# Kernel optimization log

Measured on AMD Instinct MI355X. Metric: run time of the kernel, lower is better.

The kernel has to match this reference:

```python
import jax, jax.numpy as jnp
import numpy as np

NUM_SLOTS = 64
MEMORY_DIM = 512
EMBED_DIM = 1024
SCALE = MEMORY_DIM ** (-0.5)


def setup_inputs() -> dict:
    key = jax.random.key(0)
    ks = jax.random.split(key, 7)
    B, S, E, Dm = 8, 4096, EMBED_DIM, MEMORY_DIM
    s = 0.02
    return {
        "embeddings": jax.random.normal(ks[0], (B, S, E), dtype=jnp.float32),
        "W_write": jax.random.normal(ks[1], (E, Dm), dtype=jnp.float32) * s,
        "b_write": jnp.zeros((Dm,), dtype=jnp.float32),
        "W_query": jax.random.normal(ks[2], (E, Dm), dtype=jnp.float32) * s,
        "b_query": jnp.zeros((Dm,), dtype=jnp.float32),
        "W_out": jax.random.normal(ks[3], (Dm, E), dtype=jnp.float32) * s,
        "b_out": jnp.zeros((E,), dtype=jnp.float32),
    }


def reference(embeddings, W_write, b_write, W_query, b_query, W_out, b_out):
    B, S, E = embeddings.shape
    M, Dm = NUM_SLOTS, MEMORY_DIM
    # Precompute per-token projections (linear, so identical to per-step).
    write_vals = jnp.einsum('bse,ed->bsd', embeddings, W_write) + b_write  # [B,S,Dm]
    queries = jnp.einsum('bse,ed->bsd', embeddings, W_query) + b_query      # [B,S,Dm]
    addrs = jnp.arange(S) % M  # hash(position) = position % M

    def step(carry, xs):
        memory, written = carry            # [B,M,Dm], [B,M] bool
        q, wv, addr = xs                   # [B,Dm], [B,Dm], scalar int
        # read BEFORE write (current token not yet in memory)
        sim = jnp.einsum('bd,bmd->bm', q, memory) * SCALE
        sim = jnp.where(written, sim, -jnp.inf)
        attn = jax.nn.softmax(sim, axis=-1)
        attn = jnp.nan_to_num(attn)        # all-unwritten -> zeros
        retrieved = jnp.einsum('bm,bmd->bd', attn, memory)
        memory = memory.at[:, addr, :].set(wv)
        written = written.at[:, addr].set(True)
        return (memory, written), retrieved

    mem0 = jnp.zeros((B, M, Dm), dtype=embeddings.dtype)
    wr0 = jnp.zeros((B, M), dtype=bool)
    xs = (queries.transpose(1, 0, 2), write_vals.transpose(1, 0, 2), addrs)
    _, retrieved = jax.lax.scan(step, (mem0, wr0), xs)  # [S,B,Dm]
    retrieved = retrieved.transpose(1, 0, 2)            # [B,S,Dm]
    # read_out is linear per-step -> apply once over the whole sequence
    return jnp.einsum('bsd,de->bse', retrieved, W_out) + b_out
```

## Files before the change

kernel.cpp:

```cpp
#include <hip/hip_runtime.h>
#include <hip/hip_bf16.h>
#include <math.h>


#define BATCH   8
#define S_LEN   4096
#define EMB     1024
#define DM      512
#define MROWS   (BATCH * S_LEN)
#define SCALE_F 0.04419417382415922f

typedef __attribute__((ext_vector_type(4))) float f32x4;
typedef __attribute__((ext_vector_type(8))) short short8;

__device__ __forceinline__ unsigned short f2bf(float f) {
    __hip_bfloat16 h = __float2bfloat16(f);
    return *reinterpret_cast<unsigned short*>(&h);
}

__global__ __launch_bounds__(256) void prep(
    const float4* __restrict__ emb4, ushort4* __restrict__ embb4,
    const float* __restrict__ W_wr, const float* __restrict__ W_qr,
    const float* __restrict__ W_out,
    const float* __restrict__ b_wr, const float* __restrict__ b_qr,
    __hip_bfloat16* __restrict__ wcat, __hip_bfloat16* __restrict__ wout,
    float* __restrict__ bcat)
{
    const int bx = blockIdx.x;
    if (bx < 32768) {
        int id = bx * 256 + threadIdx.x;
        float4 v = emb4[id];
        ushort4 o;
        o.x = f2bf(v.x); o.y = f2bf(v.y); o.z = f2bf(v.z); o.w = f2bf(v.w);
        embb4[id] = o;
    } else if (bx < 32768 + 2048) {
        int id = (bx - 32768) * 256 + threadIdx.x;
        int n = id >> 10, k = id & 1023;
        wcat[id] = __float2bfloat16(W_wr[k * 512 + n]);
    } else if (bx < 32768 + 4096) {
        int id = (bx - 32768 - 2048) * 256 + threadIdx.x;
        int n = id >> 10, k = id & 1023;
        wcat[(size_t)DM * EMB + id] = __float2bfloat16(W_qr[k * 512 + n]);
    } else if (bx < 32768 + 6144) {
        int id = (bx - 32768 - 4096) * 256 + threadIdx.x;
        int n = id >> 9, k = id & 511;
        wout[id] = __float2bfloat16(W_out[k * 1024 + n]);
    } else {
        int i = threadIdx.x;
#pragma unroll
        for (int r = 0; r < 4; ++r, i += 256)
            bcat[i] = (i < 512) ? b_wr[i] : b_qr[i - 512];
    }
}

template<bool BF16OUT>
__global__ __launch_bounds__(512, 2) void gemm256(
    const __hip_bfloat16* __restrict__ A, int lda,
    const __hip_bfloat16* __restrict__ Bt, int ldb,
    const float* __restrict__ bias,
    void* __restrict__ Cv, int ldc,
    int K, int nbx)
{
    __shared__ __align__(16) char smem[131072];

    const int nwg = gridDim.x;
    const int bid = blockIdx.x;
    const int cpx = nwg >> 3;
    const int swz = (bid & 7) * cpx + (bid >> 3);
    const int bm0 = (swz / nbx) << 8;
    const int bn0 = (swz % nbx) << 8;

    const int tid  = threadIdx.x;
    const int lane = tid & 63;
    const int w    = tid >> 6;
    const int wm   = w >> 2, wn = w & 3;
    const int l15  = lane & 15, lhi = lane >> 4;
    const int nt   = K >> 6;

    const int r64 = tid >> 3;
    const int cg8 = ((tid & 7) ^ (r64 & 7)) << 3;

    auto stage_tile = [&](int buf, int kt) {
#pragma unroll
        for (int h = 0; h < 4; ++h) {
            const int isB = h >> 1, hh = h & 1;
            const __hip_bfloat16* G = isB ? Bt : A;
            const int ldg = isB ? ldb : lda;
            const int rb  = (isB ? bn0 : bm0) + hh * 128;
#pragma unroll
            for (int i = 0; i < 2; ++i) {
                const __hip_bfloat16* g =
                    G + (size_t)(rb + i * 64 + r64) * ldg + kt + cg8;
                char* l = smem + buf * 65536 + isB * 32768 + hh * 16384
                          + i * 8192 + w * 1024;
                __builtin_amdgcn_global_load_lds(
                    (const __attribute__((address_space(1))) unsigned int*)g,
                    (__attribute__((address_space(3))) unsigned int*)l, 16, 0, 0);
            }
        }
    };

    f32x4 acc[8][4] = {};

    stage_tile(0, 0);
    __syncthreads();

    for (int t = 0; t < nt; ++t) {
        const int cur = t & 1;
        const bool pf = (t + 1 < nt);
        if (pf) stage_tile(cur ^ 1, (t + 1) << 6);

        const char* sA = smem + cur * 65536;
        const char* sB = sA + 32768;

        short8 bfv[2][2][2];
#pragma unroll
        for (int nh = 0; nh < 2; ++nh)
#pragma unroll
            for (int ni = 0; ni < 2; ++ni) {
                const int r = wn * 64 + nh * 32 + ni * 16 + l15;
#pragma unroll
                for (int kk = 0; kk < 2; ++kk) {
                    const int pc = (kk * 4 + lhi) ^ (r & 7);
                    bfv[nh][ni][kk] = *(const short8*)(sB + r * 128 + (pc << 4));
                }
            }

#pragma unroll
        for (int mh = 0; mh < 2; ++mh) {
            short8 af[4][2];
#pragma unroll
            for (int mi = 0; mi < 4; ++mi) {
                const int r = wm * 128 + mh * 64 + mi * 16 + l15;
#pragma unroll
                for (int kk = 0; kk < 2; ++kk) {
                    const int pc = (kk * 4 + lhi) ^ (r & 7);
                    af[mi][kk] = *(const short8*)(sA + r * 128 + (pc << 4));
                }
            }
#pragma unroll
            for (int nh = 0; nh < 2; ++nh)
#pragma unroll
                for (int mi = 0; mi < 4; ++mi)
#pragma unroll
                    for (int ni = 0; ni < 2; ++ni)
#pragma unroll
                        for (int kk = 0; kk < 2; ++kk)
                            acc[mh * 4 + mi][nh * 2 + ni] =
                                __builtin_amdgcn_mfma_f32_16x16x32_bf16(
                                    af[mi][kk], bfv[nh][ni][kk],
                                    acc[mh * 4 + mi][nh * 2 + ni], 0, 0, 0);
        }

        if (pf) __syncthreads();
    }

    float bv[4];
#pragma unroll
    for (int N = 0; N < 4; ++N)
        bv[N] = bias[bn0 + wn * 64 + (N >> 1) * 32 + (N & 1) * 16 + l15];

#pragma unroll
    for (int M = 0; M < 8; ++M)
#pragma unroll
        for (int N = 0; N < 4; ++N)
#pragma unroll
            for (int reg = 0; reg < 4; ++reg) {
                int row = bm0 + wm * 128 + (M >> 2) * 64 + (M & 3) * 16
                          + lhi * 4 + reg;
                int col = bn0 + wn * 64 + (N >> 1) * 32 + (N & 1) * 16 + l15;
                float v = acc[M][N][reg] + bv[N];
                if (BF16OUT)
                    ((__hip_bfloat16*)Cv)[(size_t)row * ldc + col] = __float2bfloat16(v);
                else
                    ((float*)Cv)[(size_t)row * ldc + col] = v;
            }
}

__global__ __launch_bounds__(256) void transpose_wv(
    const unsigned short* __restrict__ wvq,
    unsigned short* __restrict__ wvt)
{
    __shared__ unsigned short tl[64][66];
    const int tx  = blockIdx.x;
    const int dx  = blockIdx.y;
    const int b   = blockIdx.z;
    const int tid = threadIdx.x;
    const int r   = tid >> 3;
    const int c8  = (tid & 7) * 8;
    const size_t bbase = (size_t)b << 12;

#pragma unroll
    for (int it = 0; it < 2; ++it) {
        int row = r + it * 32;
        uint4 v = *(const uint4*)(wvq + ((bbase + tx * 64 + row) << 10) + dx * 64 + c8);
        *(unsigned*)&tl[row][c8 + 0] = v.x;
        *(unsigned*)&tl[row][c8 + 2] = v.y;
        *(unsigned*)&tl[row][c8 + 4] = v.z;
        *(unsigned*)&tl[row][c8 + 6] = v.w;
    }
    __syncthreads();
#pragma unroll
    for (int it = 0; it < 2; ++it) {
        int drow = r + it * 32;
        union { unsigned short s[8]; uint4 v; } o;
#pragma unroll
        for (int k = 0; k < 8; ++k) o.s[k] = tl[c8 + k][drow];
        *(uint4*)(wvt + (((size_t)b * 512 + dx * 64 + drow) << 12) + tx * 64 + c8) = o.v;
    }
}

__global__ __launch_bounds__(256) void attn_mfma(
    const __hip_bfloat16* __restrict__ WVQ,
    const __hip_bfloat16* __restrict__ WVT,
    __hip_bfloat16* __restrict__ R)
{
    __shared__ __align__(16) unsigned short p_lds[64][136];

    const int blk = blockIdx.x;
    const int b   = blk >> 6;
    const int t0  = (blk & 63) << 6;
    const int jmin = (t0 == 0) ? 64 : 0;
    const size_t bbase = (size_t)b << 12;
    const int tid  = threadIdx.x;
    const int lane = tid & 63;
    const int w    = tid >> 6;
    const int l15  = lane & 15;
    const int lhi  = lane >> 4;

    f32x4 acc[8] = {};
    const __hip_bfloat16* q0 =
        WVQ + ((bbase + t0 + w * 16 + l15) << 10) + 512 + lhi * 8;

    const __hip_bfloat16* brow[8];
#pragma unroll
    for (int nt = 0; nt < 8; ++nt) {
        int aj = t0 - 64 + nt * 16 + l15;
        if (aj < 0) aj = 0;
        brow[nt] = WVQ + ((bbase + aj) << 10) + lhi * 8;
    }

#pragma unroll 2
    for (int kt = 0; kt < 16; ++kt) {
        short8 qa = *(const short8*)(q0 + kt * 32);
#pragma unroll
        for (int nt = 0; nt < 8; ++nt) {
            short8 bv = *(const short8*)(brow[nt] + kt * 32);
            acc[nt] = __builtin_amdgcn_mfma_f32_16x16x32_bf16(qa, bv, acc[nt], 0, 0, 0);
        }
    }

    float m4[4] = { -1e30f, -1e30f, -1e30f, -1e30f };
#pragma unroll
    for (int nt = 0; nt < 8; ++nt)
#pragma unroll
        for (int reg = 0; reg < 4; ++reg) {
            int i = w * 16 + lhi * 4 + reg;
            int j = nt * 16 + l15;
            bool valid = (j >= i) && (j <= i + 63) && (j >= jmin);
            float s = valid ? acc[nt][reg] * SCALE_F : -1e30f;
            acc[nt][reg] = s;
            m4[reg] = fmaxf(m4[reg], s);
        }
#pragma unroll
    for (int off = 8; off >= 1; off >>= 1)
#pragma unroll
        for (int reg = 0; reg < 4; ++reg)
            m4[reg] = fmaxf(m4[reg], __shfl_xor(m4[reg], off, 64));

    float sum4[4] = {};
#pragma unroll
    for (int nt = 0; nt < 8; ++nt)
#pragma unroll
        for (int reg = 0; reg < 4; ++reg) {
            float s = acc[nt][reg];
            float p = (s > -1e29f) ? __expf(s - m4[reg]) : 0.f;
            acc[nt][reg] = p;
            sum4[reg] += p;
        }
#pragma unroll
    for (int off = 8; off >= 1; off >>= 1)
#pragma unroll
        for (int reg = 0; reg < 4; ++reg)
            sum4[reg] += __shfl_xor(sum4[reg], off, 64);

    float rs4[4];
#pragma unroll
    for (int reg = 0; reg < 4; ++reg)
        rs4[reg] = (sum4[reg] > 0.f) ? 1.f / sum4[reg] : 0.f;

#pragma unroll
    for (int nt = 0; nt < 8; ++nt)
#pragma unroll
        for (int reg = 0; reg < 4; ++reg)
            p_lds[w * 16 + lhi * 4 + reg][nt * 16 + l15] =
                f2bf(acc[nt][reg] * rs4[reg]);

    __syncthreads();

    short8 pa[4];
#pragma unroll
    for (int kt = 0; kt < 4; ++kt)
        pa[kt] = *(const short8*)&p_lds[w * 16 + l15][kt * 32 + lhi * 8];

    int tclamp[4];
#pragma unroll
    for (int kt = 0; kt < 4; ++kt) {
        int ti = t0 - 64 + kt * 32 + lhi * 8;
        tclamp[kt] = ti < 0 ? 0 : ti;
    }

    const size_t vbase = (size_t)b * 512;
#pragma unroll 2
    for (int nt = 0; nt < 32; ++nt) {
        int d = nt * 16 + l15;
        f32x4 a = {};
#pragma unroll
        for (int kt = 0; kt < 4; ++kt) {
            short8 bv = *(const short8*)(WVT + ((vbase + d) << 12) + tclamp[kt]);
            a = __builtin_amdgcn_mfma_f32_16x16x32_bf16(pa[kt], bv, a, 0, 0, 0);
        }
        size_t rb = (bbase + t0 + w * 16 + lhi * 4) << 9;
#pragma unroll
        for (int reg = 0; reg < 4; ++reg)
            R[rb + ((size_t)reg << 9) + d] = __float2bfloat16(a[reg]);
    }
}

extern "C" void kernel_launch(void* const* d_in, const int* in_sizes, int n_in,
                              void* d_out, int out_size, void* d_ws, size_t ws_size,
                              hipStream_t stream)
{
    const float* emb   = (const float*)d_in[0];
    const float* W_wr  = (const float*)d_in[1];
    const float* b_wr  = (const float*)d_in[2];
    const float* W_qr  = (const float*)d_in[3];
    const float* b_qr  = (const float*)d_in[4];
    const float* W_out = (const float*)d_in[5];
    const float* b_out = (const float*)d_in[6];
    float* out = (float*)d_out;

    char* ws = (char*)d_ws;
    __hip_bfloat16* embb = (__hip_bfloat16*)(ws);
    __hip_bfloat16* wvt  = (__hip_bfloat16*)(ws);
    __hip_bfloat16* wvq  = (__hip_bfloat16*)(ws + (((size_t)64) << 20));
    __hip_bfloat16* rbuf = (__hip_bfloat16*)(ws + (((size_t)128) << 20));
    __hip_bfloat16* wcat = (__hip_bfloat16*)(ws + (((size_t)160) << 20));
    __hip_bfloat16* wout = (__hip_bfloat16*)(ws + (((size_t)162) << 20));
    float*          bcat = (float*)        (ws + (((size_t)163) << 20));

    prep<<<dim3(38913), dim3(256), 0, stream>>>(
        (const float4*)emb, (ushort4*)embb,
        W_wr, W_qr, W_out, b_wr, b_qr, wcat, wout, bcat);

    gemm256<true><<<dim3(512), dim3(512), 0, stream>>>(
        embb, EMB, wcat, EMB, bcat, (void*)wvq, 1024, EMB, 4);

    transpose_wv<<<dim3(64, 8, 8), dim3(256), 0, stream>>>(
        (const unsigned short*)wvq, (unsigned short*)wvt);

    attn_mfma<<<dim3(MROWS / 64), dim3(256), 0, stream>>>(wvq, wvt, rbuf);

    gemm256<false><<<dim3(512), dim3(512), 0, stream>>>(
        rbuf, DM, wout, DM, b_out, (void*)out, EMB, DM, 4);
}
```

Measured before the change: 238.2 us.

## Fuse write-value transpose into projection GEMM epilogue and swizzle attention blocks

The projection GEMM epilogue now also writes a transposed bf16 copy of the write-value half (columns below 512), so the separate transpose kernel is removed. Each lane stores four consecutive rows as one 8-byte write into the [B,Dm,S] buffer. That saves a launch and a full read/write pass over the write values, at the cost of scattered small stores in the GEMM epilogue. The attention kernel also remaps block indices so that consecutive blocks are spread across batches, and the workspace buffers are reassigned so rbuf overlays the embedding buffer.

```diff
diff --git a/kernel.cpp b/kernel.cpp
--- a/kernel.cpp
+++ b/kernel.cpp
@@ -53,12 +53,13 @@
     }
 }
 
-template<bool BF16OUT>
+template<bool BF16OUT, bool TRANSLO>
 __global__ __launch_bounds__(512, 2) void gemm256(
     const __hip_bfloat16* __restrict__ A, int lda,
     const __hip_bfloat16* __restrict__ Bt, int ldb,
     const float* __restrict__ bias,
     void* __restrict__ Cv, int ldc,
+    __hip_bfloat16* __restrict__ wvtp,
     int K, int nbx)
 {
     __shared__ __align__(16) char smem[131072];
@@ -161,52 +162,33 @@
         bv[N] = bias[bn0 + wn * 64 + (N >> 1) * 32 + (N & 1) * 16 + l15];
 
 #pragma unroll
-    for (int M = 0; M < 8; ++M)
-#pragma unroll
-        for (int N = 0; N < 4; ++N)
+    for (int M = 0; M < 8; ++M) {
+        const int row = bm0 + wm * 128 + (M >> 2) * 64 + (M & 3) * 16 + lhi * 4;
+#pragma unroll
+        for (int N = 0; N < 4; ++N) {
+            const int col = bn0 + wn * 64 + (N >> 1) * 32 + (N & 1) * 16 + l15;
+            float v[4];
+#pragma unroll
+            for (int reg = 0; reg < 4; ++reg)
+                v[reg] = acc[M][N][reg] + bv[N];
+
 #pragma unroll
             for (int reg = 0; reg < 4; ++reg) {
-                int row = bm0 + wm * 128 + (M >> 2) * 64 + (M & 3) * 16
-                          + lhi * 4 + reg;
-                int col = bn0 + wn * 64 + (N >> 1) * 32 + (N & 1) * 16 + l15;
-                float v = acc[M][N][reg] + bv[N];
                 if (BF16OUT)
-                    ((__hip_bfloat16*)Cv)[(size_t)row * ldc + col] = __float2bfloat16(v);
+                    ((__hip_bfloat16*)Cv)[(size_t)(row + reg) * ldc + col] =
+                        __float2bfloat16(v[reg]);
                 else
-                    ((float*)Cv)[(size_t)row * ldc + col] = v;
-            }
-}
-
-__global__ __launch_bounds__(256) void transpose_wv(
-    const unsigned short* __restrict__ wvq,
-    unsigned short* __restrict__ wvt)
-{
-    __shared__ unsigned short tl[64][66];
-    const int tx  = blockIdx.x;
-    const int dx  = blockIdx.y;
-    const int b   = blockIdx.z;
-    const int tid = threadIdx.x;
-    const int r   = tid >> 3;
-    const int c8  = (tid & 7) * 8;
-    const size_t bbase = (size_t)b << 12;
-
-#pragma unroll
-    for (int it = 0; it < 2; ++it) {
-        int row = r + it * 32;
-        uint4 v = *(const uint4*)(wvq + ((bbase + tx * 64 + row) << 10) + dx * 64 + c8);
-        *(unsigned*)&tl[row][c8 + 0] = v.x;
-        *(unsigned*)&tl[row][c8 + 2] = v.y;
-        *(unsigned*)&tl[row][c8 + 4] = v.z;
-        *(unsigned*)&tl[row][c8 + 6] = v.w;
-    }
-    __syncthreads();
-#pragma unroll
-    for (int it = 0; it < 2; ++it) {
-        int drow = r + it * 32;
-        union { unsigned short s[8]; uint4 v; } o;
-#pragma unroll
-        for (int k = 0; k < 8; ++k) o.s[k] = tl[c8 + k][drow];
-        *(uint4*)(wvt + (((size_t)b * 512 + dx * 64 + drow) << 12) + tx * 64 + c8) = o.v;
+                    ((float*)Cv)[(size_t)(row + reg) * ldc + col] = v[reg];
+            }
+            if (TRANSLO && col < 512) {
+                union { unsigned short s[4]; uint2 u; } tv;
+#pragma unroll
+                for (int reg = 0; reg < 4; ++reg) tv.s[reg] = f2bf(v[reg]);
+                *(uint2*)((unsigned short*)wvtp
+                          + (((size_t)((row >> 12) * 512 + col)) << 12)
+                          + (row & 4095)) = tv.u;
+            }
+        }
     }
 }
 
@@ -217,7 +199,8 @@
 {
     __shared__ __align__(16) unsigned short p_lds[64][136];
 
-    const int blk = blockIdx.x;
+    const int blk0 = blockIdx.x;
+    const int blk  = (blk0 & 7) * 64 + (blk0 >> 3);
     const int b   = blk >> 6;
     const int t0  = (blk & 63) << 6;
     const int jmin = (t0 == 0) ? 64 : 0;
@@ -342,9 +325,9 @@
 
     char* ws = (char*)d_ws;
     __hip_bfloat16* embb = (__hip_bfloat16*)(ws);
-    __hip_bfloat16* wvt  = (__hip_bfloat16*)(ws);
+    __hip_bfloat16* rbuf = (__hip_bfloat16*)(ws);
     __hip_bfloat16* wvq  = (__hip_bfloat16*)(ws + (((size_t)64) << 20));
-    __hip_bfloat16* rbuf = (__hip_bfloat16*)(ws + (((size_t)128) << 20));
+    __hip_bfloat16* wvt  = (__hip_bfloat16*)(ws + (((size_t)128) << 20));
     __hip_bfloat16* wcat = (__hip_bfloat16*)(ws + (((size_t)160) << 20));
     __hip_bfloat16* wout = (__hip_bfloat16*)(ws + (((size_t)162) << 20));
     float*          bcat = (float*)        (ws + (((size_t)163) << 20));
@@ -353,14 +336,11 @@
         (const float4*)emb, (ushort4*)embb,
         W_wr, W_qr, W_out, b_wr, b_qr, wcat, wout, bcat);
 
-    gemm256<true><<<dim3(512), dim3(512), 0, stream>>>(
-        embb, EMB, wcat, EMB, bcat, (void*)wvq, 1024, EMB, 4);
-
-    transpose_wv<<<dim3(64, 8, 8), dim3(256), 0, stream>>>(
-        (const unsigned short*)wvq, (unsigned short*)wvt);
+    gemm256<true, true><<<dim3(512), dim3(512), 0, stream>>>(
+        embb, EMB, wcat, EMB, bcat, (void*)wvq, 1024, wvt, EMB, 4);
 
     attn_mfma<<<dim3(MROWS / 64), dim3(256), 0, stream>>>(wvq, wvt, rbuf);
 
-    gemm256<false><<<dim3(512), dim3(512), 0, stream>>>(
-        rbuf, DM, wout, DM, b_out, (void*)out, EMB, DM, 4);
-}
+    gemm256<false, false><<<dim3(512), dim3(512), 0, stream>>>(
+        rbuf, DM, wout, DM, b_out, (void*)out, EMB, nullptr, DM, 4);
+}
```

New measurement: 238.3 us. No clear change (+0.1%).
